# Performance work log

Hardware: AMD Instinct MI355X
Metric: run time of the kernel (lower is better)

The kernel has to match this reference:

```python
import jax, jax.numpy as jnp
import numpy as np

B, N, C = 4, 1024, 1024
H = 16
D = C // H  # 64
HID = int(int(C * 4.0) * 2 / 3)  # 2730
EPS = 1e-6


def rmsnorm(x, w):
    return x * jax.lax.rsqrt(jnp.mean(x * x, axis=-1, keepdims=True) + EPS) * w


def rope_cos_sin(n, d):
    inv_freq = 1.0 / (10000.0 ** (jnp.arange(0, d, 2, dtype=jnp.float32) / d))
    t = jnp.arange(n, dtype=jnp.float32)
    freqs = jnp.einsum('i,j->ij', t, inv_freq)  # [N, D/2]
    emb = jnp.concatenate([freqs, freqs], axis=-1)  # [N, D]
    return jnp.cos(emb), jnp.sin(emb)


def rotate_half(x):
    x1, x2 = jnp.split(x, 2, axis=-1)
    return jnp.concatenate([-x2, x1], axis=-1)


def setup_inputs() -> dict:
    key = jax.random.key(0)
    ks = jax.random.split(key, 12)
    s = lambda fan_in: 1.0 / np.sqrt(fan_in)
    return {
        'x': jax.random.normal(ks[0], (B, N, C), jnp.float32),
        'c': jax.random.normal(ks[1], (B, C), jnp.float32),
        'norm1_w': jnp.ones((C,), jnp.float32),
        'norm2_w': jnp.ones((C,), jnp.float32),
        'qkv_w': jax.random.normal(ks[2], (C, 3 * C), jnp.float32) * s(C),
        'proj_w': jax.random.normal(ks[3], (C, C), jnp.float32) * s(C),
        'proj_b': jnp.zeros((C,), jnp.float32),
        'qn_w': jnp.ones((D,), jnp.float32),
        'kn_w': jnp.ones((D,), jnp.float32),
        'w1': jax.random.normal(ks[4], (C, HID), jnp.float32) * s(C),
        'w2': jax.random.normal(ks[5], (HID, C), jnp.float32) * s(HID),
        'w3': jax.random.normal(ks[6], (C, HID), jnp.float32) * s(C),
        'ada_w': jax.random.normal(ks[7], (C, 6 * C), jnp.float32) * s(C),
        'ada_b': jnp.zeros((6 * C,), jnp.float32),
    }


def reference(x, c, norm1_w, norm2_w, qkv_w, proj_w, proj_b, qn_w, kn_w, w1, w2, w3, ada_w, ada_b):
    # AdaLN modulation params from conditioning
    mods = jax.nn.silu(c) @ ada_w + ada_b  # [B, 6C]
    sh_msa, sc_msa, g_msa, sh_mlp, sc_mlp, g_mlp = jnp.split(mods, 6, axis=-1)

    # --- attention branch ---
    x_mod = rmsnorm(x, norm1_w) * (1 + sc_msa[:, None, :]) + sh_msa[:, None, :]
    qkv = (x_mod @ qkv_w).reshape(B, N, 3, H, D).transpose(2, 0, 3, 1, 4)  # [3,B,H,N,D]
    q, k, v = qkv[0], qkv[1], qkv[2]
    q = rmsnorm(q, qn_w)
    k = rmsnorm(k, kn_w)
    cos, sin = rope_cos_sin(N, D)  # [N, D]
    q = q * cos + rotate_half(q) * sin
    k = k * cos + rotate_half(k) * sin
    attn = jax.nn.softmax(jnp.einsum('bhqd,bhkd->bhqk', q, k) * (D ** -0.5), axis=-1)
    o = jnp.einsum('bhqk,bhkd->bhqd', attn, v).transpose(0, 2, 1, 3).reshape(B, N, C)
    x = x + g_msa[:, None, :] * (o @ proj_w + proj_b)

    # --- SwiGLU MLP branch ---
    x_mod = rmsnorm(x, norm2_w) * (1 + sc_mlp[:, None, :]) + sh_mlp[:, None, :]
    mlp = (jax.nn.silu(x_mod @ w1) * (x_mod @ w3)) @ w2
    x = x + g_mlp[:, None, :] * mlp
    return x
```

## Files before the change

### kernel.cpp

```cpp
#include <hip/hip_runtime.h>
#include <hip/hip_bf16.h>
#include <stdint.h>

using bf16 = __hip_bfloat16;
using bf16x8 = __attribute__((ext_vector_type(8))) short;
using f32x4  = __attribute__((ext_vector_type(4))) float;
using short4v = __attribute__((ext_vector_type(4))) short;

#define EPSF 1e-6f
#define LOG2E 1.44269504088896f

__device__ __forceinline__ unsigned short f2bu(float x) {
  union { bf16 h; unsigned short u; } cvt;
  cvt.h = __float2bfloat16(x);
  return cvt.u;
}

typedef __attribute__((address_space(3))) void as3_void;
typedef const __attribute__((address_space(1))) void as1_void;

__device__ __forceinline__ void gload_lds16(const void* g, void* l) {
  as1_void* gp = (as1_void*)(uintptr_t)g;
  as3_void* lp = (as3_void*)(uint32_t)(uintptr_t)l;
  __builtin_amdgcn_global_load_lds(gp, lp, 16, 0, 0);
}

__global__ void __launch_bounds__(256) preamble(const float* __restrict__ qkvw,
                                                const float* __restrict__ projw,
                                                const float* __restrict__ w1,
                                                const float* __restrict__ w3,
                                                const float* __restrict__ w2,
                                                bf16* __restrict__ qkvwt,
                                                bf16* __restrict__ projwt,
                                                bf16* __restrict__ w1t,
                                                bf16* __restrict__ w3t,
                                                bf16* __restrict__ w2t,
                                                const float* __restrict__ cc,
                                                const float* __restrict__ adaw,
                                                float* __restrict__ part,
                                                float* __restrict__ cosT,
                                                float* __restrict__ sinT) {
  __shared__ float tile[32][33];
  __shared__ float sc[256];
  __shared__ float red[1024];
  int id = blockIdx.x;
  const int t = threadIdx.x;
  if (id < 12416) {
    const float* src; bf16* dst; int R, Cc, ldd, nbx;
    if (id < 3072)      { src = qkvw;  dst = qkvwt;  R = 1024; Cc = 3072; ldd = 1024; nbx = 96; }
    else if ((id -= 3072) < 1024) { src = projw; dst = projwt; R = 1024; Cc = 1024; ldd = 1024; nbx = 32; }
    else if ((id -= 1024) < 2752) { src = w1;    dst = w1t;    R = 1024; Cc = 2730; ldd = 1024; nbx = 86; }
    else if ((id -= 2752) < 2752) { src = w3;    dst = w3t;    R = 1024; Cc = 2730; ldd = 1024; nbx = 86; }
    else                { id -= 2752; src = w2;    dst = w2t;    R = 2730; Cc = 1024; ldd = 2816; nbx = 32; }
    const int bx = id % nbx, by = id / nbx;
    const int tx = t & 31, ty = t >> 5;
    const int ct = bx * 32, rt = by * 32;
#pragma unroll
    for (int kk = 0; kk < 4; ++kk) {
      const int r = rt + ty + kk * 8;
      float v = 0.f;
      if (r < R && (ct + tx) < Cc) v = src[(size_t)r * Cc + ct + tx];
      tile[ty + kk * 8][tx] = v;
    }
    __syncthreads();
#pragma unroll
    for (int kk = 0; kk < 4; ++kk) {
      const int c = ct + ty + kk * 8;
      const int r = rt + tx;
      if (c < Cc && r < ldd) dst[(size_t)c * ldd + r] = __float2bfloat16(tile[tx][ty + kk * 8]);
    }
  } else if ((id -= 12416) < 768) {
    const int cb = id % 48, ks = id / 48;
    const int k0 = ks * 64;
    {
      const int b = t >> 6, kk = t & 63;
      const float v = cc[b * 1024 + k0 + kk];
      sc[t] = v / (1.f + __expf(-v));
    }
    __syncthreads();
    const int colL = t & 127, kh = t >> 7;
    const int col = cb * 128 + colL;
    float a0 = 0.f, a1 = 0.f, a2 = 0.f, a3 = 0.f;
    const float* ap = adaw + (size_t)(k0 + kh * 32) * 6144 + col;
#pragma unroll
    for (int k = 0; k < 32; ++k) {
      const float awv = ap[(size_t)k * 6144];
      const int kk = kh * 32 + k;
      a0 += sc[kk] * awv; a1 += sc[64 + kk] * awv;
      a2 += sc[128 + kk] * awv; a3 += sc[192 + kk] * awv;
    }
    red[kh * 512 + 0 * 128 + colL] = a0;
    red[kh * 512 + 1 * 128 + colL] = a1;
    red[kh * 512 + 2 * 128 + colL] = a2;
    red[kh * 512 + 3 * 128 + colL] = a3;
    __syncthreads();
    if (kh == 0) {
#pragma unroll
      for (int b = 0; b < 4; ++b) {
        const float s = red[b * 128 + colL] + red[512 + b * 128 + colL];
        part[(size_t)(ks * 4 + b) * 6144 + col] = s;
      }
    }
  } else {
    id -= 768;
    const int i = id * 256 + t;
    const int n = i >> 5, fi = i & 31;
    const float invf = powf(10000.f, -(float)fi * (1.f / 32.f));
    const float ang = (float)n * invf;
    cosT[i] = cosf(ang);
    sinT[i] = sinf(ang);
  }
}

__global__ void __launch_bounds__(256) ada_reduce(const float* __restrict__ part,
                                                  const float* __restrict__ adab,
                                                  float* __restrict__ mods) {
  const int i = blockIdx.x * 256 + threadIdx.x;
  const int b = i / 6144, col = i % 6144;
  float s = adab[col];
#pragma unroll
  for (int ks = 0; ks < 16; ++ks) s += part[(size_t)(ks * 4 + b) * 6144 + col];
  mods[b * 6144 + col] = s;
}

__global__ void __launch_bounds__(256) norm_mod(const float* __restrict__ X,
                                                const float* __restrict__ wgt,
                                                const float* __restrict__ mods,
                                                int sh_off, int sc_off,
                                                bf16* __restrict__ Y) {
  __shared__ float red[4];
  const int row = blockIdx.x, t = threadIdx.x, l = t & 63, wv = t >> 6;
  const float4 xv = ((const float4*)(X + (size_t)row * 1024))[t];
  float ss = xv.x * xv.x + xv.y * xv.y + xv.z * xv.z + xv.w * xv.w;
#pragma unroll
  for (int off = 1; off < 64; off <<= 1) ss += __shfl_xor(ss, off);
  if (l == 0) red[wv] = ss;
  __syncthreads();
  ss = (red[0] + red[1]) + (red[2] + red[3]);
  const float rs = rsqrtf(ss * (1.f / 1024.f) + EPSF);
  const int b = row >> 10;
  const float* mb = mods + b * 6144;
  const int c0 = t * 4;
  float vals[4] = {xv.x, xv.y, xv.z, xv.w};
  short4v yv;
#pragma unroll
  for (int j = 0; j < 4; j++) {
    const int cc = c0 + j;
    const float y = vals[j] * rs * wgt[cc] * (1.f + mb[sc_off + cc]) + mb[sh_off + cc];
    yv[j] = (short)f2bu(y);
  }
  *(short4v*)(Y + (size_t)row * 1024 + c0) = yv;
}

template <int TN, int EPI>
__global__ void __launch_bounds__(256, 3) gemm_p(const bf16* __restrict__ A, int lda,
                                                 const bf16* __restrict__ Bt, int ldb,
                                                 int K, int Nreal, int ldc,
                                                 bf16* __restrict__ outb,
                                                 float* __restrict__ outf,
                                                 const float* __restrict__ resid,
                                                 const float* __restrict__ gate,
                                                 const float* __restrict__ bias) {
  constexpr int BUFSZ = 8192 + TN * 64;
  constexpr int WN = (TN == 128) ? 2 : 1;
  constexpr int MI = (TN == 128) ? 4 : 2;
  constexpr int WTM = (TN == 128) ? 64 : 32;
  __shared__ char smB[3 * BUFSZ];
  const int t = threadIdx.x, l = t & 63, w = t >> 6;
  const int g = l >> 4, cl = l & 15;
  const int cpx = gridDim.x >> 3;
  const int wg = blockIdx.x;
  const int swz0 = (wg & 7) * cpx + (wg >> 3);
  const int m0 = (swz0 & 31) * 128, n0 = (swz0 >> 5) * TN;
  const int wm = w / WN, wn = w % WN;
  f32x4 acc[MI][4] = {};
  const int NK = K >> 5;
  const int srow = t >> 2;
  const int scol = (((t & 3) ^ ((t >> 3) & 3))) * 8;
  const int rsw = (cl >> 1) & 3;

  auto stage = [&](int kt, int buf) {
    char* dst = smB + buf * BUFSZ;
    const int kk = kt * 32 + scol;
    gload_lds16(A + (size_t)(m0 + srow) * lda + kk,      dst + t * 16);
    gload_lds16(A + (size_t)(m0 + 64 + srow) * lda + kk, dst + 4096 + t * 16);
    gload_lds16(Bt + (size_t)(n0 + srow) * ldb + kk,     dst + 8192 + t * 16);
    if constexpr (TN == 128)
      gload_lds16(Bt + (size_t)(n0 + 64 + srow) * ldb + kk, dst + 12288 + t * 16);
  };

  stage(0, 0);
  stage(1, 1);
  if constexpr (TN == 128) asm volatile("s_waitcnt vmcnt(4)" ::: "memory");
  else                     asm volatile("s_waitcnt vmcnt(3)" ::: "memory");
  __builtin_amdgcn_s_barrier();
  __builtin_amdgcn_sched_barrier(0);
  int cur = 0;
  for (int kt = 0; kt < NK; ++kt) {
    if (kt + 2 < NK) stage(kt + 2, (cur >= 1) ? cur - 1 : 2);
    const bf16* Ab = (const bf16*)(smB + cur * BUFSZ);
    const bf16* Bb = (const bf16*)(smB + cur * BUFSZ + 8192);
    bf16x8 af[MI], bfr[4];
#pragma unroll
    for (int i = 0; i < MI; i++)
      af[i] = *(const bf16x8*)&Ab[(wm * WTM + i * 16 + cl) * 32 + ((g ^ rsw) << 3)];
#pragma unroll
    for (int i = 0; i < 4; i++)
      bfr[i] = *(const bf16x8*)&Bb[(wn * 64 + i * 16 + cl) * 32 + ((g ^ rsw) << 3)];
    __builtin_amdgcn_s_setprio(1);
#pragma unroll
    for (int mi = 0; mi < MI; mi++)
#pragma unroll
      for (int ni = 0; ni < 4; ni++)
        acc[mi][ni] = __builtin_amdgcn_mfma_f32_16x16x32_bf16(af[mi], bfr[ni], acc[mi][ni], 0, 0, 0);
    __builtin_amdgcn_s_setprio(0);
    if (kt + 2 < NK) {
      if constexpr (TN == 128) asm volatile("s_waitcnt vmcnt(4)" ::: "memory");
      else                     asm volatile("s_waitcnt vmcnt(3)" ::: "memory");
    } else {
      asm volatile("s_waitcnt vmcnt(0)" ::: "memory");
    }
    __builtin_amdgcn_s_barrier();
    __builtin_amdgcn_sched_barrier(0);
    cur = (cur + 1 == 3) ? 0 : cur + 1;
  }
#pragma unroll
  for (int mi = 0; mi < MI; mi++) {
#pragma unroll
    for (int ni = 0; ni < 4; ni++) {
      const int c = n0 + wn * 64 + ni * 16 + cl;
#pragma unroll
      for (int j = 0; j < 4; j++) {
        const int r = m0 + wm * WTM + mi * 16 + g * 4 + j;
        const float v = acc[mi][ni][j];
        if constexpr (EPI == 0) {
          if (c < Nreal) outb[(size_t)r * ldc + c] = __float2bfloat16(v);
        } else if constexpr (EPI == 1) {
          const int b = r >> 10;
          outf[(size_t)r * ldc + c] = resid[(size_t)r * ldc + c] + gate[b * 6144 + c] * (v + bias[c]);
        } else if constexpr (EPI == 4) {
          const int b = r >> 10;
          outf[(size_t)r * ldc + c] = resid[(size_t)r * ldc + c] + gate[b * 6144 + c] * v;
        }
      }
    }
  }
}

__global__ void __launch_bounds__(256, 3) gemm_qkv(const bf16* __restrict__ A, int lda,
                                                   const bf16* __restrict__ Bt, int ldb,
                                                   const float* __restrict__ cosT,
                                                   const float* __restrict__ sinT,
                                                   const float* __restrict__ qnw,
                                                   const float* __restrict__ knw,
                                                   bf16* __restrict__ Qo,
                                                   bf16* __restrict__ Ko,
                                                   bf16* __restrict__ vbt) {
  constexpr int BUFSZ = 16384;
  __shared__ char smB[3 * BUFSZ];
  const int t = threadIdx.x, l = t & 63, w = t >> 6;
  const int g = l >> 4, cl = l & 15;
  const int cpx = gridDim.x >> 3;
  const int wg = blockIdx.x;
  const int swz0 = (wg & 7) * cpx + (wg >> 3);
  const int m0 = (swz0 & 31) * 128, n0 = (swz0 >> 5) * 128;
  const int wm = w >> 1, wn = w & 1;
  f32x4 acc[4][4] = {};
  const int srow = t >> 2;
  const int scol = (((t & 3) ^ ((t >> 3) & 3))) * 8;
  const int rsw = (cl >> 1) & 3;

  auto stage = [&](int kt, int buf) {
    char* dst = smB + buf * BUFSZ;
    const int kk = kt * 32 + scol;
    gload_lds16(A + (size_t)(m0 + srow) * lda + kk,       dst + t * 16);
    gload_lds16(A + (size_t)(m0 + 64 + srow) * lda + kk,  dst + 4096 + t * 16);
    gload_lds16(Bt + (size_t)(n0 + srow) * ldb + kk,      dst + 8192 + t * 16);
    gload_lds16(Bt + (size_t)(n0 + 64 + srow) * ldb + kk, dst + 12288 + t * 16);
  };

  stage(0, 0);
  stage(1, 1);
  asm volatile("s_waitcnt vmcnt(4)" ::: "memory");
  __builtin_amdgcn_s_barrier();
  __builtin_amdgcn_sched_barrier(0);
  int cur = 0;
  for (int kt = 0; kt < 32; ++kt) {
    if (kt + 2 < 32) stage(kt + 2, (cur >= 1) ? cur - 1 : 2);
    const bf16* Ab = (const bf16*)(smB + cur * BUFSZ);
    const bf16* Bb = (const bf16*)(smB + cur * BUFSZ + 8192);
    bf16x8 af[4], bfr[4];
#pragma unroll
    for (int i = 0; i < 4; i++)
      af[i] = *(const bf16x8*)&Ab[(wm * 64 + i * 16 + cl) * 32 + ((g ^ rsw) << 3)];
#pragma unroll
    for (int i = 0; i < 4; i++)
      bfr[i] = *(const bf16x8*)&Bb[(wn * 64 + i * 16 + cl) * 32 + ((g ^ rsw) << 3)];
    __builtin_amdgcn_s_setprio(1);
#pragma unroll
    for (int mi = 0; mi < 4; mi++)
#pragma unroll
      for (int ni = 0; ni < 4; ni++)
        acc[mi][ni] = __builtin_amdgcn_mfma_f32_16x16x32_bf16(af[mi], bfr[ni], acc[mi][ni], 0, 0, 0);
    __builtin_amdgcn_s_setprio(0);
    if (kt + 2 < 32) asm volatile("s_waitcnt vmcnt(4)" ::: "memory");
    else             asm volatile("s_waitcnt vmcnt(0)" ::: "memory");
    __builtin_amdgcn_s_barrier();
    __builtin_amdgcn_sched_barrier(0);
    cur = (cur + 1 == 3) ? 0 : cur + 1;
  }

  float* cosS = (float*)smB;
  float* sinS = (float*)(smB + 16384);
  const int nb0 = m0 & 1023;
  for (int i = t; i < 4096; i += 256) {
    cosS[i] = cosT[(nb0 + (i >> 5)) * 32 + (i & 31)];
    sinS[i] = sinT[(nb0 + (i >> 5)) * 32 + (i & 31)];
  }
  __syncthreads();

  const int hb = n0 + wn * 64;
  const int type = hb >> 10;
  const int h = (hb & 1023) >> 6;
  const int b = m0 >> 10;
  const int bh = b * 16 + h;

  if (type == 2) {
#pragma unroll
    for (int mi = 0; mi < 4; mi++) {
      const int r0 = m0 + wm * 64 + mi * 16 + g * 4;
      const int nn0 = r0 & 1023;
#pragma unroll
      for (int ni = 0; ni < 4; ni++) {
        const int d = ni * 16 + cl;
        short4v pv;
#pragma unroll
        for (int j = 0; j < 4; j++) pv[j] = (short)f2bu(acc[mi][ni][j]);
        *(short4v*)(vbt + (size_t)bh * 65536 + (size_t)d * 1024 + nn0) = pv;
      }
    }
  } else {
    bf16* dst = (type == 0) ? Qo : Ko;
    const float* nwp = (type == 0) ? qnw : knw;
    const float scale = (type == 0) ? 0.125f * LOG2E : 1.f;
    float wv[4];
#pragma unroll
    for (int ni = 0; ni < 4; ni++) wv[ni] = nwp[ni * 16 + cl];
#pragma unroll
    for (int mi = 0; mi < 4; mi++) {
#pragma unroll
      for (int j = 0; j < 4; j++) {
        float ssq = 0.f;
#pragma unroll
        for (int ni = 0; ni < 4; ni++) ssq += acc[mi][ni][j] * acc[mi][ni][j];
        ssq += __shfl_xor(ssq, 1);
        ssq += __shfl_xor(ssq, 2);
        ssq += __shfl_xor(ssq, 4);
        ssq += __shfl_xor(ssq, 8);
        const float rsn = rsqrtf(ssq * (1.f / 64.f) + EPSF);
        const int r = m0 + wm * 64 + mi * 16 + g * 4 + j;
        const int nn = r & 1023, rr = r - m0;
        float vn[4];
#pragma unroll
        for (int ni = 0; ni < 4; ni++) vn[ni] = acc[mi][ni][j] * rsn * wv[ni];
        const float cs0 = cosS[rr * 32 + cl],      sn0 = sinS[rr * 32 + cl];
        const float cs1 = cosS[rr * 32 + 16 + cl], sn1 = sinS[rr * 32 + 16 + cl];
        const float o0 = (vn[0] * cs0 - vn[2] * sn0) * scale;
        const float o1 = (vn[1] * cs1 - vn[3] * sn1) * scale;
        const float o2 = (vn[2] * cs0 + vn[0] * sn0) * scale;
        const float o3 = (vn[3] * cs1 + vn[1] * sn1) * scale;
        const size_t base = ((size_t)bh * 1024 + nn) * 64;
        dst[base + cl] = __float2bfloat16(o0);
        dst[base + 16 + cl] = __float2bfloat16(o1);
        dst[base + 32 + cl] = __float2bfloat16(o2);
        dst[base + 48 + cl] = __float2bfloat16(o3);
      }
    }
  }
}

__global__ void __launch_bounds__(256, 2) gemm_dual(const bf16* __restrict__ A, int lda,
                                                    const bf16* __restrict__ B1t,
                                                    const bf16* __restrict__ B3t, int ldb,
                                                    int K, int Nreal, int ldc,
                                                    bf16* __restrict__ outb) {
  constexpr int BUFSZ = 24576;
  __shared__ char smB[2 * BUFSZ];
  const int t = threadIdx.x, l = t & 63, w = t >> 6;
  const int g = l >> 4, cl = l & 15;
  const int cpx = gridDim.x >> 3;
  const int wg = blockIdx.x;
  const int swz0 = (wg & 7) * cpx + (wg >> 3);
  const int m0 = (swz0 & 31) * 128, n0 = (swz0 >> 5) * 128;
  const int wm = w >> 1, wn = w & 1;
  f32x4 acc1[4][4] = {}, acc3[4][4] = {};
  const int NK = K >> 5;
  const int srow = t >> 2;
  const int scol = (((t & 3) ^ ((t >> 3) & 3))) * 8;
  const int rsw = (cl >> 1) & 3;

  auto stage = [&](int kt, int buf) {
    char* dst = smB + buf * BUFSZ;
    const int kk = kt * 32 + scol;
    gload_lds16(A   + (size_t)(m0 + srow) * lda + kk,      dst + t * 16);
    gload_lds16(A   + (size_t)(m0 + 64 + srow) * lda + kk, dst + 4096 + t * 16);
    gload_lds16(B1t + (size_t)(n0 + srow) * ldb + kk,      dst + 8192 + t * 16);
    gload_lds16(B1t + (size_t)(n0 + 64 + srow) * ldb + kk, dst + 12288 + t * 16);
    gload_lds16(B3t + (size_t)(n0 + srow) * ldb + kk,      dst + 16384 + t * 16);
    gload_lds16(B3t + (size_t)(n0 + 64 + srow) * ldb + kk, dst + 20480 + t * 16);
  };

  stage(0, 0);
  for (int kt = 0; kt < NK; ++kt) {
    if (kt + 1 < NK) {
      stage(kt + 1, (kt + 1) & 1);
      asm volatile("s_waitcnt vmcnt(6)" ::: "memory");
    } else {
      asm volatile("s_waitcnt vmcnt(0)" ::: "memory");
    }
    __builtin_amdgcn_s_barrier();
    __builtin_amdgcn_sched_barrier(0);
    const bf16* Ab  = (const bf16*)(smB + (kt & 1) * BUFSZ);
    const bf16* B1b = (const bf16*)(smB + (kt & 1) * BUFSZ + 8192);
    const bf16* B3b = (const bf16*)(smB + (kt & 1) * BUFSZ + 16384);
    bf16x8 af[4], b1r[4], b3r[4];
#pragma unroll
    for (int i = 0; i < 4; i++)
      af[i] = *(const bf16x8*)&Ab[(wm * 64 + i * 16 + cl) * 32 + ((g ^ rsw) << 3)];
#pragma unroll
    for (int i = 0; i < 4; i++) {
      b1r[i] = *(const bf16x8*)&B1b[(wn * 64 + i * 16 + cl) * 32 + ((g ^ rsw) << 3)];
      b3r[i] = *(const bf16x8*)&B3b[(wn * 64 + i * 16 + cl) * 32 + ((g ^ rsw) << 3)];
    }
    __builtin_amdgcn_s_setprio(1);
#pragma unroll
    for (int mi = 0; mi < 4; mi++)
#pragma unroll
      for (int ni = 0; ni < 4; ni++) {
        acc1[mi][ni] = __builtin_amdgcn_mfma_f32_16x16x32_bf16(af[mi], b1r[ni], acc1[mi][ni], 0, 0, 0);
        acc3[mi][ni] = __builtin_amdgcn_mfma_f32_16x16x32_bf16(af[mi], b3r[ni], acc3[mi][ni], 0, 0, 0);
      }
    __builtin_amdgcn_s_setprio(0);
    __builtin_amdgcn_s_barrier();
    __builtin_amdgcn_sched_barrier(0);
  }
#pragma unroll
  for (int mi = 0; mi < 4; mi++) {
#pragma unroll
    for (int ni = 0; ni < 4; ni++) {
      const int c = n0 + wn * 64 + ni * 16 + cl;
#pragma unroll
      for (int j = 0; j < 4; j++) {
        const int r = m0 + wm * 64 + mi * 16 + g * 4 + j;
        if (c < Nreal) {
          const float hv = acc1[mi][ni][j];
          const float sl = hv / (1.f + __expf(-hv));
          outb[(size_t)r * ldc + c] = __float2bfloat16(sl * acc3[mi][ni][j]);
        } else {
          outb[(size_t)r * ldc + c] = __float2bfloat16(0.f);
        }
      }
    }
  }
}

__global__ void __launch_bounds__(512) attn_fwd(const bf16* __restrict__ Qb,
                                                const bf16* __restrict__ Kb,
                                                const bf16* __restrict__ Vb,
                                                bf16* __restrict__ Ob) {
  __shared__ char KsB[2 * 8192];
  __shared__ char VsB[2 * 8192];
  __shared__ unsigned short Ps[8 * 16 * 64];
  const int t = threadIdx.x, l = t & 63, w = t >> 6;
  const int g = l >> 4, cl = l & 15;
  const int wg = blockIdx.x;
  const int bh = wg & 63;
  const int q0 = (wg >> 6) * 128;
  const bf16* Qg = Qb + (size_t)bh * 65536;
  const bf16* Kg = Kb + (size_t)bh * 65536;
  const bf16* Vg = Vb + (size_t)bh * 65536;
  const int qrow = q0 + w * 16 + cl;
  const bf16x8 aq0 = *(const bf16x8*)(Qg + (size_t)qrow * 64 + g * 8);
  const bf16x8 aq1 = *(const bf16x8*)(Qg + (size_t)qrow * 64 + 32 + g * 8);
  float mreg = -1e30f, lreg = 0.f;
  f32x4 o[4] = {};
  const int kr_l = t >> 3;
  const int ku = (t & 7) ^ ((t >> 3) & 7);
  unsigned short* Pw = Ps + w * 1024;
  const int sxor = cl & 7;

  auto stageKV = [&](int kvt, int buf) {
    const int kv0 = kvt * 64;
    gload_lds16(Kg + (size_t)(kv0 + kr_l) * 64 + ku * 8, KsB + buf * 8192 + w * 1024);
    gload_lds16(Vg + (size_t)kr_l * 1024 + kv0 + ku * 8, VsB + buf * 8192 + w * 1024);
  };

  stageKV(0, 0);
  for (int kvt = 0; kvt < 16; ++kvt) {
    const int cb = kvt & 1;
    if (kvt + 1 < 16) {
      stageKV(kvt + 1, cb ^ 1);
      asm volatile("s_waitcnt vmcnt(2)" ::: "memory");
    } else {
      asm volatile("s_waitcnt vmcnt(0)" ::: "memory");
    }
    __builtin_amdgcn_s_barrier();
    __builtin_amdgcn_sched_barrier(0);
    const char* Kt = KsB + cb * 8192;
    const char* Vt = VsB + cb * 8192;
    f32x4 s[4] = {};
#pragma unroll
    for (int ch = 0; ch < 4; ch++) {
      const int rb = (16 * ch + cl) << 7;
      const bf16x8 bk0 = *(const bf16x8*)(Kt + rb + ((g ^ sxor) << 4));
      s[ch] = __builtin_amdgcn_mfma_f32_16x16x32_bf16(bk0, aq0, s[ch], 0, 0, 0);
      const bf16x8 bk1 = *(const bf16x8*)(Kt + rb + (((4 + g) ^ sxor) << 4));
      s[ch] = __builtin_amdgcn_mfma_f32_16x16x32_bf16(bk1, aq1, s[ch], 0, 0, 0);
    }
    float pm = fmaxf(fmaxf(fmaxf(s[0][0], s[0][1]), fmaxf(s[0][2], s[0][3])),
                     fmaxf(fmaxf(s[1][0], s[1][1]), fmaxf(s[1][2], s[1][3])));
    pm = fmaxf(pm, fmaxf(fmaxf(fmaxf(s[2][0], s[2][1]), fmaxf(s[2][2], s[2][3])),
                         fmaxf(fmaxf(s[3][0], s[3][1]), fmaxf(s[3][2], s[3][3]))));
    pm = fmaxf(pm, __shfl_xor(pm, 16));
    pm = fmaxf(pm, __shfl_xor(pm, 32));
    if (!__all(pm - mreg <= 8.f)) {
      const float nm = fmaxf(mreg, pm);
      const float al = exp2f(mreg - nm);
      mreg = nm;
      lreg *= al;
#pragma unroll
      for (int dc = 0; dc < 4; dc++) {
        o[dc][0] *= al; o[dc][1] *= al; o[dc][2] *= al; o[dc][3] *= al;
      }
    }
    float rs = 0.f;
#pragma unroll
    for (int ch = 0; ch < 4; ch++) {
      const float p0 = exp2f(s[ch][0] - mreg);
      const float p1 = exp2f(s[ch][1] - mreg);
      const float p2 = exp2f(s[ch][2] - mreg);
      const float p3 = exp2f(s[ch][3] - mreg);
      rs += (p0 + p1) + (p2 + p3);
      short4v pk;
      pk[0] = (short)f2bu(p0); pk[1] = (short)f2bu(p1);
      pk[2] = (short)f2bu(p2); pk[3] = (short)f2bu(p3);
      const int phys = (2 * ch + (g >> 1)) ^ sxor;
      *(short4v*)&Pw[cl * 64 + phys * 8 + 4 * (g & 1)] = pk;
    }
    rs += __shfl_xor(rs, 16);
    rs += __shfl_xor(rs, 32);
    lreg += rs;
    const bf16x8 pa0 = *(const bf16x8*)&Pw[cl * 64 + ((g ^ sxor) << 3)];
    const bf16x8 pa1 = *(const bf16x8*)&Pw[cl * 64 + (((4 + g) ^ sxor) << 3)];
#pragma unroll
    for (int dc = 0; dc < 4; dc++) {
      const int vr = (16 * dc + cl) << 7;
      const bf16x8 bv0 = *(const bf16x8*)(Vt + vr + ((g ^ sxor) << 4));
      o[dc] = __builtin_amdgcn_mfma_f32_16x16x32_bf16(bv0, pa0, o[dc], 0, 0, 0);
      const bf16x8 bv1 = *(const bf16x8*)(Vt + vr + (((4 + g) ^ sxor) << 4));
      o[dc] = __builtin_amdgcn_mfma_f32_16x16x32_bf16(bv1, pa1, o[dc], 0, 0, 0);
    }
    __builtin_amdgcn_s_barrier();
  }
  const int b = bh >> 4, h = bh & 15;
  const float inv = 1.f / lreg;
  const int q = q0 + w * 16 + cl;
  const size_t base = ((size_t)(b * 1024 + q) * 16 + h) * 64;
#pragma unroll
  for (int dc = 0; dc < 4; dc++) {
    short4v ov;
    ov[0] = (short)f2bu(o[dc][0] * inv);
    ov[1] = (short)f2bu(o[dc][1] * inv);
    ov[2] = (short)f2bu(o[dc][2] * inv);
    ov[3] = (short)f2bu(o[dc][3] * inv);
    *(short4v*)(Ob + base + 16 * dc + 4 * g) = ov;
  }
}

extern "C" void kernel_launch(void* const* d_in, const int* in_sizes, int n_in,
                              void* d_out, int out_size, void* d_ws, size_t ws_size,
                              hipStream_t stream) {
  const float* x     = (const float*)d_in[0];
  const float* c     = (const float*)d_in[1];
  const float* n1w   = (const float*)d_in[2];
  const float* n2w   = (const float*)d_in[3];
  const float* qkvw  = (const float*)d_in[4];
  const float* projw = (const float*)d_in[5];
  const float* projb = (const float*)d_in[6];
  const float* qnw   = (const float*)d_in[7];
  const float* knw   = (const float*)d_in[8];
  const float* w1    = (const float*)d_in[9];
  const float* w2    = (const float*)d_in[10];
  const float* w3    = (const float*)d_in[11];
  const float* adaw  = (const float*)d_in[12];
  const float* adab  = (const float*)d_in[13];
  float* outp = (float*)d_out;
  char* ws = (char*)d_ws;
  if (ws_size < 93159424u) return;

  float* ropeC = (float*)(ws + 0);
  float* ropeS = (float*)(ws + 131072);
  float* mods  = (float*)(ws + 262144);
  bf16* xmod   = (bf16*)(ws + 360448);
  bf16* qkvwt  = (bf16*)(ws + 8749056);
  bf16* projwt = (bf16*)(ws + 15040512);
  bf16* w1t    = (bf16*)(ws + 17137664);
  bf16* w3t    = (bf16*)(ws + 22904832);
  bf16* w2t    = (bf16*)(ws + 28672000);
  float* apart = (float*)(ws + 34439168);
  bf16* qb     = (bf16*)(ws + 59604992);
  bf16* gbuf   = (bf16*)(ws + 59604992);
  bf16* kb     = (bf16*)(ws + 67993600);
  bf16* vbt    = (bf16*)(ws + 76382208);
  bf16* ob     = (bf16*)(ws + 84770816);

  preamble<<<13312, 256, 0, stream>>>(qkvw, projw, w1, w3, w2,
                                      qkvwt, projwt, w1t, w3t, w2t,
                                      c, adaw, apart, ropeC, ropeS);
  ada_reduce<<<96, 256, 0, stream>>>(apart, adab, mods);

  norm_mod<<<4096, 256, 0, stream>>>(x, n1w, mods, 0, 1024, xmod);
  gemm_qkv<<<768, 256, 0, stream>>>(xmod, 1024, qkvwt, 1024, ropeC, ropeS, qnw, knw,
                                    qb, kb, vbt);
  attn_fwd<<<512, 512, 0, stream>>>(qb, kb, vbt, ob);
  gemm_p<64, 1><<<512, 256, 0, stream>>>(ob, 1024, projwt, 1024, 1024, 1024, 1024,
                                         nullptr, outp, x, mods + 2048, projb);

  norm_mod<<<4096, 256, 0, stream>>>(outp, n2w, mods, 3072, 4096, xmod);
  gemm_dual<<<704, 256, 0, stream>>>(xmod, 1024, w1t, w3t, 1024, 1024, 2730, 2816,
                                     gbuf);
  gemm_p<64, 4><<<512, 256, 0, stream>>>(gbuf, 2816, w2t, 2816, 2816, 1024, 1024,
                                         nullptr, outp, outp, mods + 5120, nullptr);
}
```

Baseline: 231.9 us.

## Switch GEMM kernels from triple-buffered to double-buffered LDS pipelines

Replaces the three-stage LDS ring with two buffers in the projection/W2 GEMM and the QKV GEMM, prefetching only one k-tile ahead and waiting before compute each iteration. It also strips the unused TN=128 and bf16-output template variants from gemm_p. This lowers shared memory per block, at the cost of less load latency hiding and an extra barrier per k-step.

```diff
diff --git a/kernel.cpp b/kernel.cpp
--- a/kernel.cpp
+++ b/kernel.cpp
@@ -152,28 +152,23 @@
   *(short4v*)(Y + (size_t)row * 1024 + c0) = yv;
 }
 
-template <int TN, int EPI>
+template <int EPI>
 __global__ void __launch_bounds__(256, 3) gemm_p(const bf16* __restrict__ A, int lda,
                                                  const bf16* __restrict__ Bt, int ldb,
-                                                 int K, int Nreal, int ldc,
-                                                 bf16* __restrict__ outb,
+                                                 int K, int ldc,
                                                  float* __restrict__ outf,
                                                  const float* __restrict__ resid,
                                                  const float* __restrict__ gate,
                                                  const float* __restrict__ bias) {
-  constexpr int BUFSZ = 8192 + TN * 64;
-  constexpr int WN = (TN == 128) ? 2 : 1;
-  constexpr int MI = (TN == 128) ? 4 : 2;
-  constexpr int WTM = (TN == 128) ? 64 : 32;
-  __shared__ char smB[3 * BUFSZ];
+  constexpr int BUFSZ = 12288;
+  __shared__ char smB[2 * BUFSZ];
   const int t = threadIdx.x, l = t & 63, w = t >> 6;
   const int g = l >> 4, cl = l & 15;
   const int cpx = gridDim.x >> 3;
   const int wg = blockIdx.x;
   const int swz0 = (wg & 7) * cpx + (wg >> 3);
-  const int m0 = (swz0 & 31) * 128, n0 = (swz0 >> 5) * TN;
-  const int wm = w / WN, wn = w % WN;
-  f32x4 acc[MI][4] = {};
+  const int m0 = (swz0 & 31) * 128, n0 = (swz0 >> 5) * 64;
+  f32x4 acc[2][4] = {};
   const int NK = K >> 5;
   const int srow = t >> 2;
   const int scol = (((t & 3) ^ ((t >> 3) & 3))) * 8;
@@ -185,57 +180,47 @@
     gload_lds16(A + (size_t)(m0 + srow) * lda + kk,      dst + t * 16);
     gload_lds16(A + (size_t)(m0 + 64 + srow) * lda + kk, dst + 4096 + t * 16);
     gload_lds16(Bt + (size_t)(n0 + srow) * ldb + kk,     dst + 8192 + t * 16);
-    if constexpr (TN == 128)
-      gload_lds16(Bt + (size_t)(n0 + 64 + srow) * ldb + kk, dst + 12288 + t * 16);
   };
 
   stage(0, 0);
-  stage(1, 1);
-  if constexpr (TN == 128) asm volatile("s_waitcnt vmcnt(4)" ::: "memory");
-  else                     asm volatile("s_waitcnt vmcnt(3)" ::: "memory");
-  __builtin_amdgcn_s_barrier();
-  __builtin_amdgcn_sched_barrier(0);
-  int cur = 0;
   for (int kt = 0; kt < NK; ++kt) {
-    if (kt + 2 < NK) stage(kt + 2, (cur >= 1) ? cur - 1 : 2);
-    const bf16* Ab = (const bf16*)(smB + cur * BUFSZ);
-    const bf16* Bb = (const bf16*)(smB + cur * BUFSZ + 8192);
-    bf16x8 af[MI], bfr[4];
-#pragma unroll
-    for (int i = 0; i < MI; i++)
-      af[i] = *(const bf16x8*)&Ab[(wm * WTM + i * 16 + cl) * 32 + ((g ^ rsw) << 3)];
+    if (kt + 1 < NK) {
+      stage(kt + 1, (kt + 1) & 1);
+      asm volatile("s_waitcnt vmcnt(3)" ::: "memory");
+    } else {
+      asm volatile("s_waitcnt vmcnt(0)" ::: "memory");
+    }
+    __builtin_amdgcn_s_barrier();
+    __builtin_amdgcn_sched_barrier(0);
+    const bf16* Ab = (const bf16*)(smB + (kt & 1) * BUFSZ);
+    const bf16* Bb = (const bf16*)(smB + (kt & 1) * BUFSZ + 8192);
+    bf16x8 af[2], bfr[4];
+#pragma unroll
+    for (int i = 0; i < 2; i++)
+      af[i] = *(const bf16x8*)&Ab[(w * 32 + i * 16 + cl) * 32 + ((g ^ rsw) << 3)];
 #pragma unroll
     for (int i = 0; i < 4; i++)
-      bfr[i] = *(const bf16x8*)&Bb[(wn * 64 + i * 16 + cl) * 32 + ((g ^ rsw) << 3)];
+      bfr[i] = *(const bf16x8*)&Bb[(i * 16 + cl) * 32 + ((g ^ rsw) << 3)];
     __builtin_amdgcn_s_setprio(1);
 #pragma unroll
-    for (int mi = 0; mi < MI; mi++)
+    for (int mi = 0; mi < 2; mi++)
 #pragma unroll
       for (int ni = 0; ni < 4; ni++)
         acc[mi][ni] = __builtin_amdgcn_mfma_f32_16x16x32_bf16(af[mi], bfr[ni], acc[mi][ni], 0, 0, 0);
     __builtin_amdgcn_s_setprio(0);
-    if (kt + 2 < NK) {
-      if constexpr (TN == 128) asm volatile("s_waitcnt vmcnt(4)" ::: "memory");
-      else                     asm volatile("s_waitcnt vmcnt(3)" ::: "memory");
-    } else {
-      asm volatile("s_waitcnt vmcnt(0)" ::: "memory");
-    }
     __builtin_amdgcn_s_barrier();
     __builtin_amdgcn_sched_barrier(0);
-    cur = (cur + 1 == 3) ? 0 : cur + 1;
-  }
-#pragma unroll
-  for (int mi = 0; mi < MI; mi++) {
+  }
+#pragma unroll
+  for (int mi = 0; mi < 2; mi++) {
 #pragma unroll
     for (int ni = 0; ni < 4; ni++) {
-      const int c = n0 + wn * 64 + ni * 16 + cl;
+      const int c = n0 + ni * 16 + cl;
 #pragma unroll
       for (int j = 0; j < 4; j++) {
-        const int r = m0 + wm * WTM + mi * 16 + g * 4 + j;
+        const int r = m0 + w * 32 + mi * 16 + g * 4 + j;
         const float v = acc[mi][ni][j];
-        if constexpr (EPI == 0) {
-          if (c < Nreal) outb[(size_t)r * ldc + c] = __float2bfloat16(v);
-        } else if constexpr (EPI == 1) {
+        if constexpr (EPI == 1) {
           const int b = r >> 10;
           outf[(size_t)r * ldc + c] = resid[(size_t)r * ldc + c] + gate[b * 6144 + c] * (v + bias[c]);
         } else if constexpr (EPI == 4) {
@@ -257,7 +242,7 @@
                                                    bf16* __restrict__ Ko,
                                                    bf16* __restrict__ vbt) {
   constexpr int BUFSZ = 16384;
-  __shared__ char smB[3 * BUFSZ];
+  __shared__ char smB[2 * BUFSZ];
   const int t = threadIdx.x, l = t & 63, w = t >> 6;
   const int g = l >> 4, cl = l & 15;
   const int cpx = gridDim.x >> 3;
@@ -280,15 +265,17 @@
   };
 
   stage(0, 0);
-  stage(1, 1);
-  asm volatile("s_waitcnt vmcnt(4)" ::: "memory");
-  __builtin_amdgcn_s_barrier();
-  __builtin_amdgcn_sched_barrier(0);
-  int cur = 0;
   for (int kt = 0; kt < 32; ++kt) {
-    if (kt + 2 < 32) stage(kt + 2, (cur >= 1) ? cur - 1 : 2);
-    const bf16* Ab = (const bf16*)(smB + cur * BUFSZ);
-    const bf16* Bb = (const bf16*)(smB + cur * BUFSZ + 8192);
+    if (kt + 1 < 32) {
+      stage(kt + 1, (kt + 1) & 1);
+      asm volatile("s_waitcnt vmcnt(4)" ::: "memory");
+    } else {
+      asm volatile("s_waitcnt vmcnt(0)" ::: "memory");
+    }
+    __builtin_amdgcn_s_barrier();
+    __builtin_amdgcn_sched_barrier(0);
+    const bf16* Ab = (const bf16*)(smB + (kt & 1) * BUFSZ);
+    const bf16* Bb = (const bf16*)(smB + (kt & 1) * BUFSZ + 8192);
     bf16x8 af[4], bfr[4];
 #pragma unroll
     for (int i = 0; i < 4; i++)
@@ -303,11 +290,8 @@
       for (int ni = 0; ni < 4; ni++)
         acc[mi][ni] = __builtin_amdgcn_mfma_f32_16x16x32_bf16(af[mi], bfr[ni], acc[mi][ni], 0, 0, 0);
     __builtin_amdgcn_s_setprio(0);
-    if (kt + 2 < 32) asm volatile("s_waitcnt vmcnt(4)" ::: "memory");
-    else             asm volatile("s_waitcnt vmcnt(0)" ::: "memory");
     __builtin_amdgcn_s_barrier();
     __builtin_amdgcn_sched_barrier(0);
-    cur = (cur + 1 == 3) ? 0 : cur + 1;
   }
 
   float* cosS = (float*)smB;
@@ -623,12 +607,12 @@
   gemm_qkv<<<768, 256, 0, stream>>>(xmod, 1024, qkvwt, 1024, ropeC, ropeS, qnw, knw,
                                     qb, kb, vbt);
   attn_fwd<<<512, 512, 0, stream>>>(qb, kb, vbt, ob);
-  gemm_p<64, 1><<<512, 256, 0, stream>>>(ob, 1024, projwt, 1024, 1024, 1024, 1024,
-                                         nullptr, outp, x, mods + 2048, projb);
+  gemm_p<1><<<512, 256, 0, stream>>>(ob, 1024, projwt, 1024, 1024, 1024,
+                                     outp, x, mods + 2048, projb);
 
   norm_mod<<<4096, 256, 0, stream>>>(outp, n2w, mods, 3072, 4096, xmod);
   gemm_dual<<<704, 256, 0, stream>>>(xmod, 1024, w1t, w3t, 1024, 1024, 2730, 2816,
                                      gbuf);
-  gemm_p<64, 4><<<512, 256, 0, stream>>>(gbuf, 2816, w2t, 2816, 2816, 1024, 1024,
-                                         nullptr, outp, outp, mods + 5120, nullptr);
-}
+  gemm_p<4><<<512, 256, 0, stream>>>(gbuf, 2816, w2t, 2816, 2816, 1024,
+                                     outp, outp, mods + 5120, nullptr);
+}
```

Result: slower. 241.4 us (+4.1%).
